# Optimization experiments

Measured on AMD Instinct MI355X. Metric: run time of the kernel, lower is better.

## Reference

```python
import math
import jax, jax.numpy as jnp
import numpy as np

N_HEADS = 16
NUM_BUCKETS = 32
MAX_DISTANCE = 128


def _relative_position_bucket(relative_positions, num_buckets=NUM_BUCKETS, max_distance=MAX_DISTANCE):
    # bidirectional=True branch of the torch helper
    ret = -relative_positions
    nb = num_buckets // 2
    sign = (ret < 0).astype(jnp.int32)
    ret = jnp.abs(ret)
    max_exact = nb // 2
    is_small = ret < max_exact
    # torch .long() truncates toward zero; values in the selected (large) branch are >= 0 so int cast matches
    large = max_exact + jnp.minimum(
        (jnp.log(ret.astype(jnp.float32) / max_exact + 1e-6)
         / math.log(max_distance / max_exact) * (nb - max_exact)).astype(jnp.int32),
        nb - max_exact - 1,
    )
    return jnp.where(is_small, ret, large) + sign * nb


def setup_inputs() -> dict:
    key = jax.random.key(0)
    k1, k2, k3, k4, k5 = jax.random.split(key, 5)
    d_model = 1024
    B, L = 2, 2048
    return {
        "query": jax.random.normal(k1, (B, L, d_model), dtype=jnp.float32),
        "Wq": jax.random.normal(k2, (d_model, d_model), dtype=jnp.float32) * 0.02,
        "Wkv": jax.random.normal(k3, (d_model, 2 * d_model), dtype=jnp.float32) * 0.02,
        "Wo": jax.random.normal(k4, (d_model, d_model), dtype=jnp.float32) * 0.02,
        "rel_bias": jax.random.normal(k5, (N_HEADS * NUM_BUCKETS, 1), dtype=jnp.float32) * 0.02,
    }


def reference(query, Wq, Wkv, Wo, rel_bias):
    B, L, D = query.shape
    H = N_HEADS
    hd = D // H
    scale = 1.0 / math.sqrt(hd)

    q = query @ Wq                      # [B, L, D]
    kv = query @ Wkv                    # [B, L, 2D]
    k, v = jnp.split(kv, 2, axis=-1)

    def split_heads(x):
        return x.reshape(B, L, H, hd).transpose(0, 2, 1, 3)  # [B, H, L, hd]

    q, k, v = map(split_heads, (q, k, v))

    scores = jnp.einsum("bhqd,bhkd->bhqk", q, k) * scale      # [B, H, L, L]

    # relative position bias
    pos = jnp.arange(L)
    rp = pos[None, :] - pos[:, None]                           # mem - ctx, [L, L]
    buckets = _relative_position_bucket(rp)                    # [L, L]
    idx = buckets[None, :, :] + (jnp.arange(H) * NUM_BUCKETS)[:, None, None]  # [H, L, L]
    bias = rel_bias[idx, 0][None]                              # [1, H, L, L]

    attn = jax.nn.softmax(scores + bias, axis=-1)
    out = jnp.einsum("bhqk,bhkd->bhqd", attn, v)               # [B, H, L, hd]
    out = out.transpose(0, 2, 1, 3).reshape(B, L, D) @ Wo      # [B, L, D]
    return out, bias
```

## Files before the change

kernel.cpp:

```cpp
#include <hip/hip_runtime.h>


typedef unsigned short u16;
typedef unsigned int u32;
typedef __attribute__((ext_vector_type(4))) float f32x4;
typedef __attribute__((ext_vector_type(8))) short bf16x8;
typedef __attribute__((ext_vector_type(4))) unsigned short u16x4;

#define MFMA16(a, b, c) __builtin_amdgcn_mfma_f32_16x16x32_bf16(a, b, c, 0, 0, 0)

static __device__ inline u16 f2bf(float f) {
    u32 x = __float_as_uint(f);
    x += 0x7fffu + ((x >> 16) & 1u);
    return (u16)(x >> 16);
}
static __device__ inline u32 pk2(float a, float b) {
    return (u32)f2bf(a) | ((u32)f2bf(b) << 16);
}

__global__ __launch_bounds__(256) void build_table(
    const float* __restrict__ rel_bias, float* __restrict__ tbl)
{
    int i = blockIdx.x * 256 + threadIdx.x;
    if (i >= 16 * 4096) return;
    int rel = (i & 4095) - 2047;
    int h = i >> 12;
    int ret = -rel;
    int sign = (ret < 0) ? 1 : 0;
    int aret = (ret < 0) ? -ret : ret;
    int bucket;
    if (aret < 8) {
        bucket = aret;
    } else {
        float v = (logf((float)aret * 0.125f + 1e-6f) / logf(16.0f)) * 8.0f;
        int iv = (int)v;
        bucket = 8 + (iv < 7 ? iv : 7);
    }
    bucket += sign * 16;
    tbl[i] = rel_bias[h * 32 + bucket];
}

__global__ __launch_bounds__(256) void convert_x(
    const float* __restrict__ X, u16* __restrict__ Xb)
{
    int i = (blockIdx.x * 256 + threadIdx.x) * 8;
    float4 a = *(const float4*)(X + i);
    float4 b = *(const float4*)(X + i + 4);
    uint4 w = { pk2(a.x, a.y), pk2(a.z, a.w), pk2(b.x, b.y), pk2(b.z, b.w) };
    *(uint4*)(Xb + i) = w;
}

__global__ __launch_bounds__(256) void transpose_w(
    const float* __restrict__ Wq, const float* __restrict__ Wkv,
    const float* __restrict__ Wo, u16* __restrict__ Wt)
{
    __shared__ u16 T[64 * 72];
    const int tid = threadIdx.x;
    const int k0 = blockIdx.x * 64;
    const int nt = blockIdx.y;
    const int n0 = nt * 64;
    const float* src; int ld, nb;
    if (n0 < 1024)      { src = Wq;  ld = 1024; nb = n0; }
    else if (n0 < 3072) { src = Wkv; ld = 2048; nb = n0 - 1024; }
    else                { src = Wo;  ld = 1024; nb = n0 - 3072; }
    const int r0 = tid >> 4, c4 = (tid & 15) * 4;
    for (int rr = 0; rr < 4; rr++) {
        int row = rr * 16 + r0;
        float4 f = *(const float4*)(src + (size_t)(k0 + row) * ld + nb + c4);
        T[(c4 + 0) * 72 + row] = f2bf(f.x);
        T[(c4 + 1) * 72 + row] = f2bf(f.y);
        T[(c4 + 2) * 72 + row] = f2bf(f.z);
        T[(c4 + 3) * 72 + row] = f2bf(f.w);
    }
    __syncthreads();
    const int n = tid >> 2, ks0 = (tid & 3) * 16;
    uint4 u0 = *(const uint4*)&T[n * 72 + ks0];
    uint4 u1 = *(const uint4*)&T[n * 72 + ks0 + 8];
    uint4* d = (uint4*)(Wt + (size_t)(n0 + n) * 1024 + k0 + ks0);
    d[0] = u0; d[1] = u1;
}

__global__ __launch_bounds__(256) void bias_fill(
    const float* __restrict__ tbl, float* __restrict__ out)
{
    const int bx = blockIdx.x;
    const int h = bx >> 11, i = bx & 2047;
    const float* tp = tbl + h * 4096 + 2047 - i;
    float* dst = out + 4194304 + ((size_t)bx << 11);
    const int j0 = threadIdx.x * 8;
    float4 v0, v1;
    v0.x = tp[j0 + 0]; v0.y = tp[j0 + 1]; v0.z = tp[j0 + 2]; v0.w = tp[j0 + 3];
    v1.x = tp[j0 + 4]; v1.y = tp[j0 + 5]; v1.z = tp[j0 + 6]; v1.w = tp[j0 + 7];
    float4* dv = (float4*)(dst + j0);
    dv[0] = v0; dv[1] = v1;
}

__global__ __launch_bounds__(256) void qkv_gemm(
    const u16* __restrict__ Xb, const u16* __restrict__ Wt,
    u16* __restrict__ qws, u16* __restrict__ kws, u16* __restrict__ vtws)
{
    __shared__ u16 As[128 * 72];
    __shared__ u16 Bs[128 * 72];
    const int tid = threadIdx.x;
    const int n0 = blockIdx.x * 128;
    const int m0 = blockIdx.y * 128;
    const int wid = tid >> 6, lane = tid & 63, c = lane & 15, quad = lane >> 4;
    const int wm = (wid >> 1) * 64, wn = (wid & 1) * 64;
    const f32x4 z = {0.f, 0.f, 0.f, 0.f};
    f32x4 acc[4][4];
    for (int i = 0; i < 4; i++) for (int j = 0; j < 4; j++) acc[i][j] = z;
    const int srow = tid >> 1, sk = (tid & 1) * 32;
    const u16* ag = Xb + (size_t)(m0 + srow) * 1024 + sk;
    const u16* bg = Wt + (size_t)(n0 + srow) * 1024 + sk;

    for (int kk = 0; kk < 1024; kk += 64) {
        uint4 a0 = *(const uint4*)(ag + kk);
        uint4 a1 = *(const uint4*)(ag + kk + 8);
        uint4 a2 = *(const uint4*)(ag + kk + 16);
        uint4 a3 = *(const uint4*)(ag + kk + 24);
        uint4 b0 = *(const uint4*)(bg + kk);
        uint4 b1 = *(const uint4*)(bg + kk + 8);
        uint4 b2 = *(const uint4*)(bg + kk + 16);
        uint4 b3 = *(const uint4*)(bg + kk + 24);
        uint4* da = (uint4*)&As[srow * 72 + sk];
        da[0] = a0; da[1] = a1; da[2] = a2; da[3] = a3;
        uint4* db = (uint4*)&Bs[srow * 72 + sk];
        db[0] = b0; db[1] = b1; db[2] = b2; db[3] = b3;
        __syncthreads();
        for (int ks = 0; ks < 2; ks++) {
            bf16x8 af[4], bfr[4];
            for (int im = 0; im < 4; im++)
                af[im] = *(const bf16x8*)&As[(wm + im * 16 + c) * 72 + ks * 32 + quad * 8];
            for (int jn = 0; jn < 4; jn++)
                bfr[jn] = *(const bf16x8*)&Bs[(wn + jn * 16 + c) * 72 + ks * 32 + quad * 8];
            for (int im = 0; im < 4; im++)
                for (int jn = 0; jn < 4; jn++)
                    acc[im][jn] = MFMA16(af[im], bfr[jn], acc[im][jn]);
        }
        __syncthreads();
    }
    for (int im = 0; im < 4; im++) for (int jn = 0; jn < 4; jn++) {
        int gm0 = m0 + wm + im * 16 + quad * 4;
        int gn = n0 + wn + jn * 16 + c;
        if (gn < 2048) {
            u16* dstbase = (gn < 1024) ? qws : kws;
            int nn = gn & 1023;
            int h = nn >> 6, d = nn & 63;
            for (int r = 0; r < 4; r++) {
                int gm = gm0 + r, bb = gm >> 11, l = gm & 2047;
                dstbase[(((size_t)bb * 16 + h) * 2048 + l) * 64 + d] = f2bf(acc[im][jn][r]);
            }
        } else {
            int nn = gn - 2048;
            int h = nn >> 6, d = nn & 63;
            int bb = gm0 >> 11, l = gm0 & 2047;
            u16x4 pk = { f2bf(acc[im][jn][0]), f2bf(acc[im][jn][1]),
                         f2bf(acc[im][jn][2]), f2bf(acc[im][jn][3]) };
            *(u16x4*)&vtws[(((size_t)bb * 16 + h) * 64 + d) * 2048 + l] = pk;
        }
    }
}

__global__ __launch_bounds__(256, 2) void attn_kernel(
    const u16* __restrict__ qws, const u16* __restrict__ kws,
    const u16* __restrict__ vtws, const float* __restrict__ tbl,
    u16* __restrict__ ows)
{
    __shared__ u16 QPs[128 * 72];
    __shared__ u16 Ks[2][64 * 72];
    __shared__ u16 Vt[2][64 * 72];
    __shared__ float Bw[2][192];
    const int tid = threadIdx.x;
    const int qt = blockIdx.x, bh = blockIdx.y;
    const int b = bh >> 4, h = bh & 15;
    const u16* qp = qws + (size_t)bh * 2048 * 64;
    const u16* kp = kws + (size_t)bh * 2048 * 64;
    const u16* vp = vtws + (size_t)bh * 64 * 2048;
    const float* tb = tbl + h * 4096;
    const int q0 = qt * 128;
    const int wid = tid >> 6, lane = tid & 63, c = lane & 15, quad = lane >> 4;
    const int qw0 = wid * 32;
    const int srow = tid >> 2, sc0 = (tid & 3) * 16;

    {
        int row = tid >> 1, c0 = (tid & 1) * 32;
        const uint4* s = (const uint4*)(qp + (size_t)(q0 + row) * 64 + c0);
        uint4 v0 = s[0], v1 = s[1], v2 = s[2], v3 = s[3];
        uint4* d = (uint4*)&QPs[row * 72 + c0];
        d[0] = v0; d[1] = v1; d[2] = v2; d[3] = v3;
    }
    {
        const uint4* s1 = (const uint4*)(kp + (size_t)srow * 64 + sc0);
        uint4 x0 = s1[0], x1 = s1[1];
        const uint4* s2 = (const uint4*)(vp + (size_t)srow * 2048 + sc0);
        uint4 y0 = s2[0], y1 = s2[1];
        *(uint4*)&Ks[0][srow * 72 + sc0] = x0;
        *(uint4*)&Ks[0][srow * 72 + sc0 + 8] = x1;
        *(uint4*)&Vt[0][srow * 72 + sc0] = y0;
        *(uint4*)&Vt[0][srow * 72 + sc0 + 8] = y1;
        if (tid < 192) Bw[0][tid] = tb[1920 - q0 + tid];
    }
    __syncthreads();
    bf16x8 bq[2][2];
    for (int nt = 0; nt < 2; nt++)
        for (int ks = 0; ks < 2; ks++)
            bq[nt][ks] = *(const bf16x8*)&QPs[(qw0 + nt * 16 + c) * 72 + ks * 32 + quad * 8];
    __syncthreads();
    u16* Ps = QPs + wid * (32 * 72);

    float lrow[2] = { 0.f, 0.f };
    const f32x4 z = {0.f, 0.f, 0.f, 0.f};
    f32x4 accO[2][4];
    for (int i = 0; i < 2; i++) for (int j = 0; j < 4; j++) accO[i][j] = z;

    for (int kt = 0; kt < 32; kt++) {
        const int cur = kt & 1, nxt = cur ^ 1;
        const int k0 = kt * 64;
        uint4 x0, x1, y0, y1; float bwv = 0.f;
        if (kt < 31) {
            const uint4* s1 = (const uint4*)(kp + (size_t)(k0 + 64 + srow) * 64 + sc0);
            x0 = s1[0]; x1 = s1[1];
            const uint4* s2 = (const uint4*)(vp + (size_t)srow * 2048 + k0 + 64 + sc0);
            y0 = s2[0]; y1 = s2[1];
            if (tid < 192) bwv = tb[k0 + 64 - q0 + 1920 + tid];
        }
        f32x4 accS[4][2];
        for (int i = 0; i < 4; i++) { accS[i][0] = z; accS[i][1] = z; }
        for (int ks = 0; ks < 2; ks++)
            for (int ktile = 0; ktile < 4; ktile++) {
                bf16x8 ak = *(const bf16x8*)&Ks[cur][(ktile * 16 + c) * 72 + ks * 32 + quad * 8];
                accS[ktile][0] = MFMA16(ak, bq[0][ks], accS[ktile][0]);
                accS[ktile][1] = MFMA16(ak, bq[1][ks], accS[ktile][1]);
            }
        float rsum[2] = { 0.f, 0.f };
        for (int ktile = 0; ktile < 4; ktile++)
            for (int nt = 0; nt < 2; nt++) {
                const float* bp = &Bw[cur][ktile * 16 + quad * 4 - qw0 - nt * 16 - c + 127];
                float p0 = __expf(fmaf(accS[ktile][nt][0], 0.125f, bp[0]));
                float p1 = __expf(fmaf(accS[ktile][nt][1], 0.125f, bp[1]));
                float p2 = __expf(fmaf(accS[ktile][nt][2], 0.125f, bp[2]));
                float p3 = __expf(fmaf(accS[ktile][nt][3], 0.125f, bp[3]));
                rsum[nt] += (p0 + p1) + (p2 + p3);
                u16x4 pk = { f2bf(p0), f2bf(p1), f2bf(p2), f2bf(p3) };
                *(u16x4*)&Ps[(nt * 16 + c) * 72 + ktile * 16 + quad * 4] = pk;
            }
        lrow[0] += rsum[0]; lrow[1] += rsum[1];
        for (int kb = 0; kb < 2; kb++) {
            bf16x8 bv[4];
            for (int nt = 0; nt < 4; nt++)
                bv[nt] = *(const bf16x8*)&Vt[cur][(nt * 16 + c) * 72 + kb * 32 + quad * 8];
            for (int mt = 0; mt < 2; mt++) {
                bf16x8 ap = *(const bf16x8*)&Ps[(mt * 16 + c) * 72 + kb * 32 + quad * 8];
                for (int nt = 0; nt < 4; nt++)
                    accO[mt][nt] = MFMA16(ap, bv[nt], accO[mt][nt]);
            }
        }
        if (kt < 31) {
            *(uint4*)&Ks[nxt][srow * 72 + sc0] = x0;
            *(uint4*)&Ks[nxt][srow * 72 + sc0 + 8] = x1;
            *(uint4*)&Vt[nxt][srow * 72 + sc0] = y0;
            *(uint4*)&Vt[nxt][srow * 72 + sc0 + 8] = y1;
            if (tid < 192) Bw[nxt][tid] = bwv;
            __syncthreads();
        }
    }
    for (int nt = 0; nt < 2; nt++) {
        lrow[nt] += __shfl_xor(lrow[nt], 16, 64);
        lrow[nt] += __shfl_xor(lrow[nt], 32, 64);
    }
    for (int mt = 0; mt < 2; mt++)
        for (int r = 0; r < 4; r++) {
            float lq = __shfl(lrow[mt], quad * 4 + r, 64);
            float rl = 1.0f / lq;
            int qg = q0 + qw0 + mt * 16 + quad * 4 + r;
            size_t base = ((size_t)b * 2048 + qg) * 1024 + h * 64;
            for (int nt = 0; nt < 4; nt++)
                ows[base + nt * 16 + c] = f2bf(accO[mt][nt][r] * rl);
        }
}

__global__ __launch_bounds__(256) void out_gemm(
    const u16* __restrict__ O, const u16* __restrict__ Wot, float* __restrict__ out)
{
    __shared__ u16 As[128 * 72];
    __shared__ u16 Bs[128 * 72];
    const int tid = threadIdx.x;
    const int n0 = blockIdx.x * 128;
    const int m0 = blockIdx.y * 128;
    const int wid = tid >> 6, lane = tid & 63, c = lane & 15, quad = lane >> 4;
    const int wm = (wid >> 1) * 64, wn = (wid & 1) * 64;
    const f32x4 z = {0.f, 0.f, 0.f, 0.f};
    f32x4 acc[4][4];
    for (int i = 0; i < 4; i++) for (int j = 0; j < 4; j++) acc[i][j] = z;
    const int srow = tid >> 1, sk = (tid & 1) * 32;
    const u16* ag = O + (size_t)(m0 + srow) * 1024 + sk;
    const u16* bg = Wot + (size_t)(n0 + srow) * 1024 + sk;
    for (int kk = 0; kk < 1024; kk += 64) {
        uint4 a0 = *(const uint4*)(ag + kk);
        uint4 a1 = *(const uint4*)(ag + kk + 8);
        uint4 a2 = *(const uint4*)(ag + kk + 16);
        uint4 a3 = *(const uint4*)(ag + kk + 24);
        uint4 b0 = *(const uint4*)(bg + kk);
        uint4 b1 = *(const uint4*)(bg + kk + 8);
        uint4 b2 = *(const uint4*)(bg + kk + 16);
        uint4 b3 = *(const uint4*)(bg + kk + 24);
        uint4* da = (uint4*)&As[srow * 72 + sk];
        da[0] = a0; da[1] = a1; da[2] = a2; da[3] = a3;
        uint4* db = (uint4*)&Bs[srow * 72 + sk];
        db[0] = b0; db[1] = b1; db[2] = b2; db[3] = b3;
        __syncthreads();
        for (int ks = 0; ks < 2; ks++) {
            bf16x8 af[4], bfr[4];
            for (int im = 0; im < 4; im++)
                af[im] = *(const bf16x8*)&As[(wm + im * 16 + c) * 72 + ks * 32 + quad * 8];
            for (int jn = 0; jn < 4; jn++)
                bfr[jn] = *(const bf16x8*)&Bs[(wn + jn * 16 + c) * 72 + ks * 32 + quad * 8];
            for (int im = 0; im < 4; im++)
                for (int jn = 0; jn < 4; jn++)
                    acc[im][jn] = MFMA16(af[im], bfr[jn], acc[im][jn]);
        }
        __syncthreads();
    }
    for (int im = 0; im < 4; im++) for (int jn = 0; jn < 4; jn++) {
        int gm0 = m0 + wm + im * 16 + quad * 4;
        int gn = n0 + wn + jn * 16 + c;
        for (int r = 0; r < 4; r++)
            out[(size_t)(gm0 + r) * 1024 + gn] = acc[im][jn][r];
    }
}

extern "C" void kernel_launch(void* const* d_in, const int* in_sizes, int n_in,
                              void* d_out, int out_size, void* d_ws, size_t ws_size,
                              hipStream_t stream)
{
    (void)in_sizes; (void)n_in; (void)out_size; (void)ws_size;
    const float* query    = (const float*)d_in[0];
    const float* Wq       = (const float*)d_in[1];
    const float* Wkv      = (const float*)d_in[2];
    const float* Wo       = (const float*)d_in[3];
    const float* rel_bias = (const float*)d_in[4];
    float* out = (float*)d_out;

    float* tbl = (float*)d_ws;
    u16* Xb   = (u16*)((char*)d_ws + 262144);
    u16* Wt   = Xb + 4194304;
    u16* qws  = Wt + 4194304;
    u16* kws  = qws + 4194304;
    u16* vtws = kws + 4194304;
    u16* ows  = vtws + 4194304;

    build_table<<<256, 256, 0, stream>>>(rel_bias, tbl);
    convert_x<<<2048, 256, 0, stream>>>(query, Xb);
    transpose_w<<<dim3(16, 64), 256, 0, stream>>>(Wq, Wkv, Wo, Wt);
    bias_fill<<<32768, 256, 0, stream>>>(tbl, out);
    qkv_gemm<<<dim3(24, 32), 256, 0, stream>>>(Xb, Wt, qws, kws, vtws);
    attn_kernel<<<dim3(16, 32), 256, 0, stream>>>(qws, kws, vtws, tbl, ows);
    out_gemm<<<dim3(8, 32), 256, 0, stream>>>(ows, Wt + (size_t)3072 * 1024, out);
}
```

Baseline: 441.0 us.

## Fuse prep kernels, write bias in attention, use direct-to-LDS swizzled GEMM loads

Merges the table build, input conversion and weight transpose into one prep kernel to cut launches. Drops the separate bias_fill pass; the attention kernel now writes the 256 MB bias output with nontemporal stores while it loops over key tiles. Both GEMMs load tiles straight into LDS with global_load_lds into an XOR-swizzled unpadded layout, avoiding a register round trip. Writing bias inside attention adds store traffic to a compute-bound kernel, and only batch 0 or 1 of each head writes a given slice (via b*32 offset), which the bias indexing depends on.

```diff
diff --git a/kernel.cpp b/kernel.cpp
--- a/kernel.cpp
+++ b/kernel.cpp
@@ -9,6 +9,12 @@
 
 #define MFMA16(a, b, c) __builtin_amdgcn_mfma_f32_16x16x32_bf16(a, b, c, 0, 0, 0)
 
+typedef const __attribute__((address_space(1))) void gvoid;
+typedef __attribute__((address_space(3))) void lvoid;
+static __device__ __forceinline__ void gll16(const void* g, void* l) {
+    __builtin_amdgcn_global_load_lds((gvoid*)g, (lvoid*)l, 16, 0, 0);
+}
+
 static __device__ inline u16 f2bf(float f) {
     u32 x = __float_as_uint(f);
     x += 0x7fffu + ((x >> 16) & 1u);
@@ -18,89 +24,69 @@
     return (u32)f2bf(a) | ((u32)f2bf(b) << 16);
 }
 
-__global__ __launch_bounds__(256) void build_table(
-    const float* __restrict__ rel_bias, float* __restrict__ tbl)
-{
-    int i = blockIdx.x * 256 + threadIdx.x;
-    if (i >= 16 * 4096) return;
-    int rel = (i & 4095) - 2047;
-    int h = i >> 12;
-    int ret = -rel;
-    int sign = (ret < 0) ? 1 : 0;
-    int aret = (ret < 0) ? -ret : ret;
-    int bucket;
-    if (aret < 8) {
-        bucket = aret;
+__global__ __launch_bounds__(256) void prep(
+    const float* __restrict__ X, const float* __restrict__ Wq,
+    const float* __restrict__ Wkv, const float* __restrict__ Wo,
+    const float* __restrict__ rel_bias, u16* __restrict__ Xb,
+    u16* __restrict__ Wt, float* __restrict__ tbl)
+{
+    __shared__ u16 T[64 * 72];
+    const int bx = blockIdx.x, tid = threadIdx.x;
+    if (bx < 2048) {
+        int i = (bx * 256 + tid) * 8;
+        float4 a = *(const float4*)(X + i);
+        float4 b = *(const float4*)(X + i + 4);
+        uint4 w = { pk2(a.x, a.y), pk2(a.z, a.w), pk2(b.x, b.y), pk2(b.z, b.w) };
+        *(uint4*)(Xb + i) = w;
+    } else if (bx < 3072) {
+        int bx2 = bx - 2048;
+        int k0 = (bx2 & 15) * 64;
+        int n0 = (bx2 >> 4) * 64;
+        const float* src; int ld, nb;
+        if (n0 < 1024)      { src = Wq;  ld = 1024; nb = n0; }
+        else if (n0 < 3072) { src = Wkv; ld = 2048; nb = n0 - 1024; }
+        else                { src = Wo;  ld = 1024; nb = n0 - 3072; }
+        const int r0 = tid >> 4, c4 = (tid & 15) * 4;
+        for (int rr = 0; rr < 4; rr++) {
+            int row = rr * 16 + r0;
+            float4 f = *(const float4*)(src + (size_t)(k0 + row) * ld + nb + c4);
+            T[(c4 + 0) * 72 + row] = f2bf(f.x);
+            T[(c4 + 1) * 72 + row] = f2bf(f.y);
+            T[(c4 + 2) * 72 + row] = f2bf(f.z);
+            T[(c4 + 3) * 72 + row] = f2bf(f.w);
+        }
+        __syncthreads();
+        const int n = tid >> 2, ks0 = (tid & 3) * 16;
+        uint4 u0 = *(const uint4*)&T[n * 72 + ks0];
+        uint4 u1 = *(const uint4*)&T[n * 72 + ks0 + 8];
+        uint4* d = (uint4*)(Wt + (size_t)(n0 + n) * 1024 + k0 + ks0);
+        d[0] = u0; d[1] = u1;
     } else {
-        float v = (logf((float)aret * 0.125f + 1e-6f) / logf(16.0f)) * 8.0f;
-        int iv = (int)v;
-        bucket = 8 + (iv < 7 ? iv : 7);
-    }
-    bucket += sign * 16;
-    tbl[i] = rel_bias[h * 32 + bucket];
-}
-
-__global__ __launch_bounds__(256) void convert_x(
-    const float* __restrict__ X, u16* __restrict__ Xb)
-{
-    int i = (blockIdx.x * 256 + threadIdx.x) * 8;
-    float4 a = *(const float4*)(X + i);
-    float4 b = *(const float4*)(X + i + 4);
-    uint4 w = { pk2(a.x, a.y), pk2(a.z, a.w), pk2(b.x, b.y), pk2(b.z, b.w) };
-    *(uint4*)(Xb + i) = w;
-}
-
-__global__ __launch_bounds__(256) void transpose_w(
-    const float* __restrict__ Wq, const float* __restrict__ Wkv,
-    const float* __restrict__ Wo, u16* __restrict__ Wt)
-{
-    __shared__ u16 T[64 * 72];
-    const int tid = threadIdx.x;
-    const int k0 = blockIdx.x * 64;
-    const int nt = blockIdx.y;
-    const int n0 = nt * 64;
-    const float* src; int ld, nb;
-    if (n0 < 1024)      { src = Wq;  ld = 1024; nb = n0; }
-    else if (n0 < 3072) { src = Wkv; ld = 2048; nb = n0 - 1024; }
-    else                { src = Wo;  ld = 1024; nb = n0 - 3072; }
-    const int r0 = tid >> 4, c4 = (tid & 15) * 4;
-    for (int rr = 0; rr < 4; rr++) {
-        int row = rr * 16 + r0;
-        float4 f = *(const float4*)(src + (size_t)(k0 + row) * ld + nb + c4);
-        T[(c4 + 0) * 72 + row] = f2bf(f.x);
-        T[(c4 + 1) * 72 + row] = f2bf(f.y);
-        T[(c4 + 2) * 72 + row] = f2bf(f.z);
-        T[(c4 + 3) * 72 + row] = f2bf(f.w);
-    }
-    __syncthreads();
-    const int n = tid >> 2, ks0 = (tid & 3) * 16;
-    uint4 u0 = *(const uint4*)&T[n * 72 + ks0];
-    uint4 u1 = *(const uint4*)&T[n * 72 + ks0 + 8];
-    uint4* d = (uint4*)(Wt + (size_t)(n0 + n) * 1024 + k0 + ks0);
-    d[0] = u0; d[1] = u1;
-}
-
-__global__ __launch_bounds__(256) void bias_fill(
-    const float* __restrict__ tbl, float* __restrict__ out)
-{
-    const int bx = blockIdx.x;
-    const int h = bx >> 11, i = bx & 2047;
-    const float* tp = tbl + h * 4096 + 2047 - i;
-    float* dst = out + 4194304 + ((size_t)bx << 11);
-    const int j0 = threadIdx.x * 8;
-    float4 v0, v1;
-    v0.x = tp[j0 + 0]; v0.y = tp[j0 + 1]; v0.z = tp[j0 + 2]; v0.w = tp[j0 + 3];
-    v1.x = tp[j0 + 4]; v1.y = tp[j0 + 5]; v1.z = tp[j0 + 6]; v1.w = tp[j0 + 7];
-    float4* dv = (float4*)(dst + j0);
-    dv[0] = v0; dv[1] = v1;
+        int i = (bx - 3072) * 256 + tid;
+        int rel = (i & 4095) - 2047;
+        int h = i >> 12;
+        int ret = -rel;
+        int sign = (ret < 0) ? 1 : 0;
+        int aret = (ret < 0) ? -ret : ret;
+        int bucket;
+        if (aret < 8) {
+            bucket = aret;
+        } else {
+            float v = (logf((float)aret * 0.125f + 1e-6f) / logf(16.0f)) * 8.0f;
+            int iv = (int)v;
+            bucket = 8 + (iv < 7 ? iv : 7);
+        }
+        bucket += sign * 16;
+        tbl[i] = rel_bias[h * 32 + bucket];
+    }
 }
 
 __global__ __launch_bounds__(256) void qkv_gemm(
     const u16* __restrict__ Xb, const u16* __restrict__ Wt,
     u16* __restrict__ qws, u16* __restrict__ kws, u16* __restrict__ vtws)
 {
-    __shared__ u16 As[128 * 72];
-    __shared__ u16 Bs[128 * 72];
+    __shared__ u16 As[128 * 64];
+    __shared__ u16 Bs[128 * 64];
     const int tid = threadIdx.x;
     const int n0 = blockIdx.x * 128;
     const int m0 = blockIdx.y * 128;
@@ -109,30 +95,27 @@
     const f32x4 z = {0.f, 0.f, 0.f, 0.f};
     f32x4 acc[4][4];
     for (int i = 0; i < 4; i++) for (int j = 0; j < 4; j++) acc[i][j] = z;
-    const int srow = tid >> 1, sk = (tid & 1) * 32;
-    const u16* ag = Xb + (size_t)(m0 + srow) * 1024 + sk;
-    const u16* bg = Wt + (size_t)(n0 + srow) * 1024 + sk;
+    const int rsub = lane >> 3;
+    const int dchunk = (lane & 7) ^ (rsub & 7);
+    const u16* ag = Xb + (size_t)(m0 + wid * 32 + rsub) * 1024 + dchunk * 8;
+    const u16* bg = Wt + (size_t)(n0 + wid * 32 + rsub) * 1024 + dchunk * 8;
+    u16* lA = &As[(wid * 32) * 64];
+    u16* lB = &Bs[(wid * 32) * 64];
+    const int sw = c & 7;
 
     for (int kk = 0; kk < 1024; kk += 64) {
-        uint4 a0 = *(const uint4*)(ag + kk);
-        uint4 a1 = *(const uint4*)(ag + kk + 8);
-        uint4 a2 = *(const uint4*)(ag + kk + 16);
-        uint4 a3 = *(const uint4*)(ag + kk + 24);
-        uint4 b0 = *(const uint4*)(bg + kk);
-        uint4 b1 = *(const uint4*)(bg + kk + 8);
-        uint4 b2 = *(const uint4*)(bg + kk + 16);
-        uint4 b3 = *(const uint4*)(bg + kk + 24);
-        uint4* da = (uint4*)&As[srow * 72 + sk];
-        da[0] = a0; da[1] = a1; da[2] = a2; da[3] = a3;
-        uint4* db = (uint4*)&Bs[srow * 72 + sk];
-        db[0] = b0; db[1] = b1; db[2] = b2; db[3] = b3;
+        for (int i = 0; i < 4; i++)
+            gll16(ag + (size_t)i * 8 * 1024 + kk, lA + i * 8 * 64);
+        for (int i = 0; i < 4; i++)
+            gll16(bg + (size_t)i * 8 * 1024 + kk, lB + i * 8 * 64);
         __syncthreads();
         for (int ks = 0; ks < 2; ks++) {
+            const int sl = ((ks * 4 + quad) ^ sw) * 8;
             bf16x8 af[4], bfr[4];
             for (int im = 0; im < 4; im++)
-                af[im] = *(const bf16x8*)&As[(wm + im * 16 + c) * 72 + ks * 32 + quad * 8];
+                af[im] = *(const bf16x8*)&As[(wm + im * 16 + c) * 64 + sl];
             for (int jn = 0; jn < 4; jn++)
-                bfr[jn] = *(const bf16x8*)&Bs[(wn + jn * 16 + c) * 72 + ks * 32 + quad * 8];
+                bfr[jn] = *(const bf16x8*)&Bs[(wn + jn * 16 + c) * 64 + sl];
             for (int im = 0; im < 4; im++)
                 for (int jn = 0; jn < 4; jn++)
                     acc[im][jn] = MFMA16(af[im], bfr[jn], acc[im][jn]);
@@ -164,7 +147,7 @@
 __global__ __launch_bounds__(256, 2) void attn_kernel(
     const u16* __restrict__ qws, const u16* __restrict__ kws,
     const u16* __restrict__ vtws, const float* __restrict__ tbl,
-    u16* __restrict__ ows)
+    u16* __restrict__ ows, float* __restrict__ bias_out)
 {
     __shared__ u16 QPs[128 * 72];
     __shared__ u16 Ks[2][64 * 72];
@@ -181,6 +164,7 @@
     const int wid = tid >> 6, lane = tid & 63, c = lane & 15, quad = lane >> 4;
     const int qw0 = wid * 32;
     const int srow = tid >> 2, sc0 = (tid & 3) * 16;
+    const int birow = tid >> 3, bjj = (tid & 7) * 4;
 
     {
         int row = tid >> 1, c0 = (tid & 1) * 32;
@@ -255,6 +239,16 @@
                     accO[mt][nt] = MFMA16(ap, bv[nt], accO[mt][nt]);
             }
         }
+        {
+            const int jbase = k0 + b * 32 + bjj;
+            const float* tw = tb + (jbase + 2047 - q0);
+            float* dstb = bias_out + ((size_t)h * 2048 + q0 + birow) * 2048 + jbase;
+            for (int rr = 0; rr < 4; rr++) {
+                const float* twp = tw - (birow + rr * 32);
+                f32x4 v = { twp[0], twp[1], twp[2], twp[3] };
+                __builtin_nontemporal_store(v, (f32x4*)(dstb + (size_t)rr * 32 * 2048));
+            }
+        }
         if (kt < 31) {
             *(uint4*)&Ks[nxt][srow * 72 + sc0] = x0;
             *(uint4*)&Ks[nxt][srow * 72 + sc0 + 8] = x1;
@@ -282,8 +276,8 @@
 __global__ __launch_bounds__(256) void out_gemm(
     const u16* __restrict__ O, const u16* __restrict__ Wot, float* __restrict__ out)
 {
-    __shared__ u16 As[128 * 72];
-    __shared__ u16 Bs[128 * 72];
+    __shared__ u16 As[128 * 64];
+    __shared__ u16 Bs[128 * 64];
     const int tid = threadIdx.x;
     const int n0 = blockIdx.x * 128;
     const int m0 = blockIdx.y * 128;
@@ -292,29 +286,26 @@
     const f32x4 z = {0.f, 0.f, 0.f, 0.f};
     f32x4 acc[4][4];
     for (int i = 0; i < 4; i++) for (int j = 0; j < 4; j++) acc[i][j] = z;
-    const int srow = tid >> 1, sk = (tid & 1) * 32;
-    const u16* ag = O + (size_t)(m0 + srow) * 1024 + sk;
-    const u16* bg = Wot + (size_t)(n0 + srow) * 1024 + sk;
+    const int rsub = lane >> 3;
+    const int dchunk = (lane & 7) ^ (rsub & 7);
+    const u16* ag = O + (size_t)(m0 + wid * 32 + rsub) * 1024 + dchunk * 8;
+    const u16* bg = Wot + (size_t)(n0 + wid * 32 + rsub) * 1024 + dchunk * 8;
+    u16* lA = &As[(wid * 32) * 64];
+    u16* lB = &Bs[(wid * 32) * 64];
+    const int sw = c & 7;
     for (int kk = 0; kk < 1024; kk += 64) {
-        uint4 a0 = *(const uint4*)(ag + kk);
-        uint4 a1 = *(const uint4*)(ag + kk + 8);
-        uint4 a2 = *(const uint4*)(ag + kk + 16);
-        uint4 a3 = *(const uint4*)(ag + kk + 24);
-        uint4 b0 = *(const uint4*)(bg + kk);
-        uint4 b1 = *(const uint4*)(bg + kk + 8);
-        uint4 b2 = *(const uint4*)(bg + kk + 16);
-        uint4 b3 = *(const uint4*)(bg + kk + 24);
-        uint4* da = (uint4*)&As[srow * 72 + sk];
-        da[0] = a0; da[1] = a1; da[2] = a2; da[3] = a3;
-        uint4* db = (uint4*)&Bs[srow * 72 + sk];
-        db[0] = b0; db[1] = b1; db[2] = b2; db[3] = b3;
+        for (int i = 0; i < 4; i++)
+            gll16(ag + (size_t)i * 8 * 1024 + kk, lA + i * 8 * 64);
+        for (int i = 0; i < 4; i++)
+            gll16(bg + (size_t)i * 8 * 1024 + kk, lB + i * 8 * 64);
         __syncthreads();
         for (int ks = 0; ks < 2; ks++) {
+            const int sl = ((ks * 4 + quad) ^ sw) * 8;
             bf16x8 af[4], bfr[4];
             for (int im = 0; im < 4; im++)
-                af[im] = *(const bf16x8*)&As[(wm + im * 16 + c) * 72 + ks * 32 + quad * 8];
+                af[im] = *(const bf16x8*)&As[(wm + im * 16 + c) * 64 + sl];
             for (int jn = 0; jn < 4; jn++)
-                bfr[jn] = *(const bf16x8*)&Bs[(wn + jn * 16 + c) * 72 + ks * 32 + quad * 8];
+                bfr[jn] = *(const bf16x8*)&Bs[(wn + jn * 16 + c) * 64 + sl];
             for (int im = 0; im < 4; im++)
                 for (int jn = 0; jn < 4; jn++)
                     acc[im][jn] = MFMA16(af[im], bfr[jn], acc[im][jn]);
@@ -325,7 +316,7 @@
         int gm0 = m0 + wm + im * 16 + quad * 4;
         int gn = n0 + wn + jn * 16 + c;
         for (int r = 0; r < 4; r++)
-            out[(size_t)(gm0 + r) * 1024 + gn] = acc[im][jn][r];
+            __builtin_nontemporal_store(acc[im][jn][r], &out[(size_t)(gm0 + r) * 1024 + gn]);
     }
 }
 
@@ -349,11 +340,9 @@
     u16* vtws = kws + 4194304;
     u16* ows  = vtws + 4194304;
 
-    build_table<<<256, 256, 0, stream>>>(rel_bias, tbl);
-    convert_x<<<2048, 256, 0, stream>>>(query, Xb);
-    transpose_w<<<dim3(16, 64), 256, 0, stream>>>(Wq, Wkv, Wo, Wt);
-    bias_fill<<<32768, 256, 0, stream>>>(tbl, out);
+    prep<<<3328, 256, 0, stream>>>(query, Wq, Wkv, Wo, rel_bias, Xb, Wt, tbl);
     qkv_gemm<<<dim3(24, 32), 256, 0, stream>>>(Xb, Wt, qws, kws, vtws);
-    attn_kernel<<<dim3(16, 32), 256, 0, stream>>>(qws, kws, vtws, tbl, ows);
+    attn_kernel<<<dim3(16, 32), 256, 0, stream>>>(qws, kws, vtws, tbl, ows,
+                                                  out + 4194304);
     out_gemm<<<dim3(8, 32), 256, 0, stream>>>(ows, Wt + (size_t)3072 * 1024, out);
 }
```

After: 401.7 us. 8.9% less time.
